# Kernel tuning notes

Hardware: AMD Instinct MI355X
Metric: run time of the kernel (lower is better)

The kernel has to match this reference:

```python
import jax, jax.numpy as jnp
import numpy as np

D = 256; HEADS = 8; LEVELS = 4; POINTS = 4; DFFN = 1024
B = 8; NQ = 300; NC = 16
SPATIAL = [(64, 64), (32, 32), (16, 16), (8, 8)]  # (H, W) per feature level (static)
LEN_IN = sum(h * w for h, w in SPATIAL)  # 5440
EPS = 1e-5


def layer_norm(x, w, b):
    m = x.mean(-1, keepdims=True)
    v = ((x - m) ** 2).mean(-1, keepdims=True)
    return (x - m) * jax.lax.rsqrt(v + EPS) * w + b


def mha(q, k, v, in_w, in_b, out_w, out_b):
    # torch nn.MultiheadAttention with packed qkv in_proj. q,k,v: [b, s, D]
    b, s, _ = q.shape
    dh = D // HEADS
    wq, wk, wv = jnp.split(in_w, 3, axis=0)
    bq, bk, bv = jnp.split(in_b, 3)
    proj = lambda x, w, bb: (x @ w.T + bb).reshape(b, s, HEADS, dh).transpose(0, 2, 1, 3)
    qh, kh, vh = proj(q, wq, bq), proj(k, wk, bk), proj(v, wv, bv)
    attn = jax.nn.softmax(jnp.einsum('bhqd,bhkd->bhqk', qh / np.sqrt(dh), kh), axis=-1)
    o = jnp.einsum('bhqk,bhkd->bhqd', attn, vh).transpose(0, 2, 1, 3).reshape(b, s, D)
    return o @ out_w.T + out_b


def bilinear_sample(value_l, loc, H_, W_):
    # value_l: [b, heads, H_*W_, dh]; loc: [b, heads, lq, P, 2] normalized to [0,1]
    # matches F.grid_sample(mode='bilinear', padding_mode='zeros', align_corners=False)
    b, nh, lq, p, _ = loc.shape
    dh = value_l.shape[-1]
    x = loc[..., 0] * W_ - 0.5
    y = loc[..., 1] * H_ - 0.5
    x0f = jnp.floor(x); y0f = jnp.floor(y)
    lx = x - x0f; ly = y - y0f
    x0 = x0f.astype(jnp.int32); y0 = y0f.astype(jnp.int32)
    def gather(xi, yi, w):
        valid = (xi >= 0) & (xi < W_) & (yi >= 0) & (yi < H_)
        idx = jnp.clip(yi, 0, H_ - 1) * W_ + jnp.clip(xi, 0, W_ - 1)
        vals = jnp.take_along_axis(value_l, idx.reshape(b, nh, lq * p, 1), axis=2)
        return vals.reshape(b, nh, lq, p, dh) * (w * valid)[..., None]
    out = gather(x0, y0, (1 - lx) * (1 - ly))
    out = out + gather(x0 + 1, y0, lx * (1 - ly))
    out = out + gather(x0, y0 + 1, (1 - lx) * ly)
    out = out + gather(x0 + 1, y0 + 1, lx * ly)
    return out  # [b, heads, lq, P, dh]


def ms_deform_attn(query, ref_pts, src, pad_mask, value_w, value_b, off_w, off_b, attw_w, attw_b, out_w, out_b):
    b, lq, _ = query.shape
    dh = D // HEADS
    value = src @ value_w.T + value_b
    value = jnp.where(pad_mask[..., None], 0.0, value)
    value = value.reshape(b, LEN_IN, HEADS, dh).transpose(0, 2, 1, 3)  # [b,H,Len,dh]
    off = (query @ off_w.T + off_b).reshape(b, lq, HEADS, LEVELS, POINTS, 2)
    aw = jax.nn.softmax((query @ attw_w.T + attw_b).reshape(b, lq, HEADS, LEVELS * POINTS), axis=-1)
    aw = aw.reshape(b, lq, HEADS, LEVELS, POINTS).transpose(0, 2, 1, 3, 4)  # [b,H,lq,L,P]
    norm = jnp.array([[w_, h_] for h_, w_ in SPATIAL], dtype=query.dtype)  # (W, H) per level
    loc = ref_pts[:, :, None, :, None, :] + off / norm[None, None, None, :, None, :]
    loc = loc.transpose(0, 2, 1, 3, 4, 5)  # [b,H,lq,L,P,2]
    out = jnp.zeros((b, HEADS, lq, dh), query.dtype)
    start = 0
    for l, (H_, W_) in enumerate(SPATIAL):
        v_l = jax.lax.dynamic_slice_in_dim(value, start, H_ * W_, axis=2)
        s = bilinear_sample(v_l, loc[:, :, :, l], H_, W_)
        out = out + (s * aw[:, :, :, l, :, None]).sum(3)
        start += H_ * W_
    out = out.transpose(0, 2, 1, 3).reshape(b, lq, D)
    return out @ out_w.T + out_b


def setup_inputs():
    ks = iter(jax.random.split(jax.random.key(0), 64))
    w = lambda *shape: jax.random.normal(next(ks), shape, jnp.float32) * 0.02
    return {
        'tgt': jax.random.normal(next(ks), (B, NQ, NC, D), jnp.float32),
        'query_pos': jax.random.normal(next(ks), (B, NQ, NC, D), jnp.float32),
        'reference_points': jax.random.uniform(next(ks), (B, NQ * NC, LEVELS, 2), jnp.float32),
        'src': jax.random.normal(next(ks), (B, LEN_IN, D), jnp.float32),
        'src_spatial_shapes': jnp.array(SPATIAL, jnp.int32),
        'level_start_index': jnp.array(np.cumsum([0] + [h * ww for h, ww in SPATIAL[:-1]]), jnp.int32),
        'src_padding_mask': jnp.zeros((B, LEN_IN), bool),
        'sa_in_w': w(3 * D, D), 'sa_in_b': jnp.zeros(3 * D, jnp.float32),
        'sa_out_w': w(D, D), 'sa_out_b': jnp.zeros(D, jnp.float32),
        'norm2_w': jnp.ones(D, jnp.float32), 'norm2_b': jnp.zeros(D, jnp.float32),
        'ca_value_w': w(D, D), 'ca_value_b': jnp.zeros(D, jnp.float32),
        'ca_off_w': w(HEADS * LEVELS * POINTS * 2, D), 'ca_off_b': w(HEADS * LEVELS * POINTS * 2),
        'ca_attw_w': w(HEADS * LEVELS * POINTS, D), 'ca_attw_b': jnp.zeros(HEADS * LEVELS * POINTS, jnp.float32),
        'ca_out_w': w(D, D), 'ca_out_b': jnp.zeros(D, jnp.float32),
        'norm1_w': jnp.ones(D, jnp.float32), 'norm1_b': jnp.zeros(D, jnp.float32),
        'lin1_w': w(DFFN, D), 'lin1_b': jnp.zeros(DFFN, jnp.float32),
        'lin2_w': w(D, DFFN), 'lin2_b': jnp.zeros(D, jnp.float32),
        'norm3_w': jnp.ones(D, jnp.float32), 'norm3_b': jnp.zeros(D, jnp.float32),
    }


def _forward(tgt, query_pos, reference_points, src, pad_mask, sa_in_w, sa_in_b, sa_out_w, sa_out_b, norm2_w, norm2_b, ca_value_w, ca_value_b, ca_off_w, ca_off_b, ca_attw_w, ca_attw_b, ca_out_w, ca_out_b, norm1_w, norm1_b, lin1_w, lin1_b, lin2_w, lin2_b, norm3_w, norm3_b):
    b, nq, nc, dm = tgt.shape
    # point-to-point self-attention within each contour (batch folded with queries)
    t = tgt.reshape(b * nq, nc, dm)
    qp = query_pos.reshape(b * nq, nc, dm)
    q = t + qp
    t2 = mha(q, q, t, sa_in_w, sa_in_b, sa_out_w, sa_out_b)
    t = layer_norm(t + t2, norm2_w, norm2_b)
    # multi-scale deformable cross-attention over flattened feature pyramid
    t = t.reshape(b, nq * nc, dm)
    qp = qp.reshape(b, nq * nc, dm)
    t2 = ms_deform_attn(t + qp, reference_points, src, pad_mask, ca_value_w, ca_value_b, ca_off_w, ca_off_b, ca_attw_w, ca_attw_b, ca_out_w, ca_out_b)
    t = layer_norm(t + t2, norm1_w, norm1_b)
    # FFN (dropout is identity in eval)
    t2 = jax.nn.relu(t @ lin1_w.T + lin1_b) @ lin2_w.T + lin2_b
    t = layer_norm(t + t2, norm3_w, norm3_b)
    return t.reshape(b, nq, nc, dm)


def reference(tgt, query_pos, reference_points, src, src_spatial_shapes, level_start_index, src_padding_mask, sa_in_w, sa_in_b, sa_out_w, sa_out_b, norm2_w, norm2_b, ca_value_w, ca_value_b, ca_off_w, ca_off_b, ca_attw_w, ca_attw_b, ca_out_w, ca_out_b, norm1_w, norm1_b, lin1_w, lin1_b, lin2_w, lin2_b, norm3_w, norm3_b):
    # src_spatial_shapes / level_start_index are static (SPATIAL); accepted for API fidelity
    return _forward(tgt, query_pos, reference_points, src, src_padding_mask, sa_in_w, sa_in_b, sa_out_w, sa_out_b, norm2_w, norm2_b, ca_value_w, ca_value_b, ca_off_w, ca_off_b, ca_attw_w, ca_attw_b, ca_out_w, ca_out_b, norm1_w, norm1_b, lin1_w, lin1_b, lin2_w, lin2_b, norm3_w, norm3_b)
```

## Files before the change

kernel.cpp:

```cpp
#include <hip/hip_runtime.h>


typedef __bf16 bf16x8 __attribute__((ext_vector_type(8)));
typedef float  f32x4  __attribute__((ext_vector_type(4)));
typedef float  f32x2  __attribute__((ext_vector_type(2)));

__device__ __forceinline__ unsigned pk_bf16(float lo, float hi)
{
    unsigned a = __float_as_uint(lo) + 0x8000u;
    unsigned b = __float_as_uint(hi) + 0x8000u;
    return __builtin_amdgcn_perm(b, a, 0x07060302u);
}
__device__ __forceinline__ unsigned short f2bf(float v)
{
    return (unsigned short)((__float_as_uint(v) + 0x8000u) >> 16);
}
__device__ __forceinline__ float bf_lo(unsigned u) { return __uint_as_float(u << 16); }
__device__ __forceinline__ float bf_hi(unsigned u) { return __uint_as_float(u & 0xffff0000u); }
__device__ __forceinline__ float bf1(unsigned short u) { return __uint_as_float((unsigned)u << 16); }
__device__ __forceinline__ f32x2 bfpair(unsigned u)
{
    f32x2 r;
    r.x = __uint_as_float(u << 16);
    r.y = __uint_as_float(u & 0xffff0000u);
    return r;
}

__device__ __forceinline__ int xcd_swz(int wgid, int nwg)
{
    const int q = nwg >> 3, r = nwg & 7;
    const int x = wgid & 7, k = wgid >> 3;
    return (x < r ? x * (q + 1) : r * (q + 1) + (x - r) * q) + k;
}

__device__ __forceinline__ void gl_lds16(const unsigned short* g, unsigned short* l)
{
    __builtin_amdgcn_global_load_lds(
        (const __attribute__((address_space(1))) unsigned int*)g,
        (__attribute__((address_space(3))) unsigned int*)l,
        16, 0, 0);
}

struct WcvtArgs {
    const float* src[8];
    unsigned short* dst[8];
    int n4[8];
};

__global__ __launch_bounds__(256) void wcvt(WcvtArgs a)
{
    const int gid = blockIdx.x * 256 + threadIdx.x;
    const int stride = gridDim.x * 256;
#pragma unroll
    for (int s = 0; s < 8; s++) {
        const float4* sp = (const float4*)a.src[s];
        uint2* dp = (uint2*)a.dst[s];
        for (int i = gid; i < a.n4[s]; i += stride) {
            float4 f = sp[i];
            uint2 o; o.x = pk_bf16(f.x, f.y); o.y = pk_bf16(f.z, f.w);
            dp[i] = o;
        }
    }
}

__global__ __launch_bounds__(256) void cvt_acts(
    const float* __restrict__ tgt, const float* __restrict__ qpos,
    const float* __restrict__ src,
    unsigned short* __restrict__ tgtB, unsigned short* __restrict__ qB,
    unsigned short* __restrict__ srcB)
{
    const int gid = blockIdx.x * 256 + threadIdx.x;
    const int stride = gridDim.x * 256;
    for (int i = gid; i < 2457600; i += stride) {
        float4 t = ((const float4*)tgt)[i];
        float4 p = ((const float4*)qpos)[i];
        uint2 a; a.x = pk_bf16(t.x, t.y); a.y = pk_bf16(t.z, t.w);
        ((uint2*)tgtB)[i] = a;
        uint2 b; b.x = pk_bf16(t.x + p.x, t.y + p.y);
        b.y = pk_bf16(t.z + p.z, t.w + p.w);
        ((uint2*)qB)[i] = b;
    }
    for (int i = gid; i < 2785280; i += stride) {
        float4 s = ((const float4*)src)[i];
        uint2 c; c.x = pk_bf16(s.x, s.y); c.y = pk_bf16(s.z, s.w);
        ((uint2*)srcB)[i] = c;
    }
}

__device__ __forceinline__ void gemm_core128(
    const unsigned short* __restrict__ Ab,
    const unsigned short* __restrict__ Wb, const float* __restrict__ bias,
    void* __restrict__ Cv, int outbf16, int relu,
    int row0, int col0, int N, int K,
    unsigned short (*sA)[128][32], unsigned short (*sB)[128][32])
{
    const int tid  = threadIdx.x;
    const int lane = tid & 63;
    const int wv   = tid >> 6;
    const int wr   = wv >> 1;
    const int wc   = wv & 1;
    const int lm   = lane & 15;
    const int q    = lane >> 4;
    const int q4   = q << 2;

    const int tr = tid >> 2;
    const int ts = tid & 3;

    f32x4 acc[4][4] = {};
    const int iters = K >> 5;

    auto stage = [&](int buf, int k) {
#pragma unroll
        for (int r = 0; r < 2; ++r) {
            const int row = r * 64 + tr;
            const int sw  = ts ^ ((row >> 1) & 3);
            gl_lds16(Ab + (size_t)(row0 + row) * K + k + sw * 8,
                     &sA[buf][0][0] + (size_t)(r * 256 + tid) * 8);
            gl_lds16(Wb + (size_t)(col0 + row) * K + k + sw * 8,
                     &sB[buf][0][0] + (size_t)(r * 256 + tid) * 8);
        }
    };

    stage(0, 0);

    for (int it = 0; it < iters; ++it) {
        __syncthreads();
        const int buf = it & 1;
        if (it + 1 < iters) stage(buf ^ 1, (it + 1) << 5);

        bf16x8 av[4], bv[4];
#pragma unroll
        for (int mi = 0; mi < 4; mi++) {
            const int row = wr * 64 + mi * 16 + lm;
            av[mi] = *(const bf16x8*)&sA[buf][row][(q ^ ((row >> 1) & 3)) * 8];
        }
#pragma unroll
        for (int ni = 0; ni < 4; ni++) {
            const int row = wc * 64 + ni * 16 + lm;
            bv[ni] = *(const bf16x8*)&sB[buf][row][(q ^ ((row >> 1) & 3)) * 8];
        }
#pragma unroll
        for (int mi = 0; mi < 4; mi++)
#pragma unroll
            for (int ni = 0; ni < 4; ni++)
                acc[mi][ni] = __builtin_amdgcn_mfma_f32_16x16x32_bf16(
                    av[mi], bv[ni], acc[mi][ni], 0, 0, 0);
    }

#pragma unroll
    for (int ni = 0; ni < 4; ni++) {
        const int col = col0 + wc * 64 + ni * 16 + lm;
        const float bsv = bias[col];
#pragma unroll
        for (int mi = 0; mi < 4; mi++) {
            const int rowb = row0 + wr * 64 + mi * 16 + q4;
#pragma unroll
            for (int rr = 0; rr < 4; rr++) {
                float v = acc[mi][ni][rr] + bsv;
                if (relu) v = fmaxf(v, 0.f);
                if (outbf16)
                    ((unsigned short*)Cv)[(size_t)(rowb + rr) * N + col] = f2bf(v);
                else
                    ((float*)Cv)[(size_t)(rowb + rr) * N + col] = v;
            }
        }
    }
}

__global__ __launch_bounds__(256) void gemm_std128(
    const unsigned short* __restrict__ Ab,
    const unsigned short* __restrict__ Wb, const float* __restrict__ bias,
    void* __restrict__ Cv, int outbf16, int relu, int N, int K)
{
    __shared__ unsigned short sA[2][128][32];
    __shared__ unsigned short sB[2][128][32];
    const int nwg = gridDim.x * gridDim.y;
    const int w = xcd_swz(blockIdx.x + gridDim.x * blockIdx.y, nwg);
    const int x = w % gridDim.x, y = w / gridDim.x;
    gemm_core128(Ab, Wb, bias, Cv, outbf16, relu,
                 y * 128, x * 128, N, K, sA, sB);
}

__global__ __launch_bounds__(256) void gemm_qkvval(
    const unsigned short* __restrict__ qB, const unsigned short* __restrict__ tgtB,
    const unsigned short* __restrict__ srcB,
    const unsigned short* __restrict__ Wsa, const float* __restrict__ bsa,
    unsigned short* __restrict__ qkB, unsigned short* __restrict__ vB,
    const unsigned short* __restrict__ Wval, const float* __restrict__ bval,
    unsigned short* __restrict__ valB)
{
    __shared__ unsigned short sA[2][128][32];
    __shared__ unsigned short sB[2][128][32];
    const int w = xcd_swz(blockIdx.x + 8 * blockIdx.y, 2720);
    const int x = w & 7, y = w >> 3;
    if (x < 4) {
        if (y >= 300) return;
        gemm_core128(qB, Wsa, bsa, qkB, 1, 0, y * 128, x * 128, 512, 256, sA, sB);
    } else if (x < 6) {
        if (y >= 300) return;
        gemm_core128(tgtB, Wsa + 512 * 256, bsa + 512, vB, 1, 0,
                     y * 128, (x - 4) * 128, 256, 256, sA, sB);
    } else {
        gemm_core128(srcB, Wval, bval, valB, 1, 0,
                     y * 128, (x - 6) * 128, 256, 256, sA, sB);
    }
}

__global__ __launch_bounds__(256) void gemm_offaw(
    const unsigned short* __restrict__ X,
    const unsigned short* __restrict__ Woff, const float* __restrict__ boff,
    unsigned short* __restrict__ offB,
    const unsigned short* __restrict__ Watt, const float* __restrict__ batt,
    float* __restrict__ awL)
{
    __shared__ unsigned short sA[2][128][32];
    __shared__ unsigned short sB[2][128][32];
    const int w = xcd_swz(blockIdx.x + 3 * blockIdx.y, 900);
    const int x = w % 3, y = w / 3;
    if (x >= 2)
        gemm_core128(X, Watt, batt, awL, 0, 0,
                     y * 128, 0, 128, 256, sA, sB);
    else
        gemm_core128(X, Woff, boff, offB, 1, 0,
                     y * 128, x * 128, 256, 256, sA, sB);
}

__global__ __launch_bounds__(256) void attn16(
    const unsigned short* __restrict__ QK, const unsigned short* __restrict__ V,
    unsigned short* __restrict__ O)
{
    __shared__ unsigned short sqk[16][520];
    __shared__ unsigned short sv[16][264];
    __shared__ float sp[128][17];

    const int g = blockIdx.x;
    const int tid = threadIdx.x;

    const uint4* qg = (const uint4*)(QK + (size_t)g * 8192);
    for (int i = tid; i < 1024; i += 256)
        *(uint4*)&sqk[i >> 6][(i & 63) * 8] = qg[i];
    const uint4* vg = (const uint4*)(V + (size_t)g * 4096);
    for (int i = tid; i < 512; i += 256)
        *(uint4*)&sv[i >> 5][(i & 31) * 8] = vg[i];
    __syncthreads();

#pragma unroll 2
    for (int s = tid; s < 2048; s += 256) {
        const int h = s >> 8, qi = (s >> 4) & 15, kj = s & 15;
        const uint4* qp = (const uint4*)&sqk[qi][h * 32];
        const uint4* kp = (const uint4*)&sqk[kj][256 + h * 32];
        float acc = 0.f;
#pragma unroll
        for (int c = 0; c < 4; c++) {
            uint4 qu = qp[c];
            uint4 ku = kp[c];
            acc += bf_lo(qu.x) * bf_lo(ku.x) + bf_hi(qu.x) * bf_hi(ku.x)
                 + bf_lo(qu.y) * bf_lo(ku.y) + bf_hi(qu.y) * bf_hi(ku.y)
                 + bf_lo(qu.z) * bf_lo(ku.z) + bf_hi(qu.z) * bf_hi(ku.z)
                 + bf_lo(qu.w) * bf_lo(ku.w) + bf_hi(qu.w) * bf_hi(ku.w);
        }
        sp[s >> 4][s & 15] = acc * 0.17677669529663687f;
    }
    __syncthreads();

    if (tid < 128) {
        float* row = sp[tid];
        float mx = row[0];
#pragma unroll
        for (int j = 1; j < 16; j++) mx = fmaxf(mx, row[j]);
        float sum = 0.f;
#pragma unroll
        for (int j = 0; j < 16; j++) { float e = __expf(row[j] - mx); row[j] = e; sum += e; }
        float inv = 1.f / sum;
#pragma unroll
        for (int j = 0; j < 16; j++) row[j] *= inv;
    }
    __syncthreads();

    uint2* og = (uint2*)(O + (size_t)g * 4096);
    for (int o = tid; o < 1024; o += 256) {
        const int qi = o >> 6, cq = o & 63, h = cq >> 3;
        const float* pr = sp[h * 16 + qi];
        float a0 = 0.f, a1 = 0.f, a2 = 0.f, a3 = 0.f;
#pragma unroll
        for (int j = 0; j < 16; j++) {
            uint2 u = *(const uint2*)&sv[j][cq * 4];
            float p = pr[j];
            a0 += p * bf_lo(u.x); a1 += p * bf_hi(u.x);
            a2 += p * bf_lo(u.y); a3 += p * bf_hi(u.y);
        }
        uint2 r; r.x = pk_bf16(a0, a1); r.y = pk_bf16(a2, a3);
        og[o] = r;
    }
}

template <int XBF16, int WRITE2, int ADDQ>
__global__ __launch_bounds__(256) void ln_res4(
    const void* __restrict__ Xv, const float* __restrict__ R,
    const float* __restrict__ w, const float* __restrict__ b,
    float* __restrict__ out, unsigned short* __restrict__ out2,
    const float* __restrict__ qpos)
{
    const int row = blockIdx.x * 4 + (threadIdx.x >> 6);
    const int lane = threadIdx.x & 63;
    const size_t base = (size_t)row * 256 + lane * 4;

    float x0, x1, x2, x3;
    if (XBF16) {
        uint2 u = *(const uint2*)((const unsigned short*)Xv + base);
        x0 = bf_lo(u.x); x1 = bf_hi(u.x); x2 = bf_lo(u.y); x3 = bf_hi(u.y);
    } else {
        float4 f = *(const float4*)((const float*)Xv + base);
        x0 = f.x; x1 = f.y; x2 = f.z; x3 = f.w;
    }
    float4 r4 = *(const float4*)&R[base];
    float v0 = x0 + r4.x, v1 = x1 + r4.y, v2 = x2 + r4.z, v3 = x3 + r4.w;

    float s = v0 + v1 + v2 + v3;
#pragma unroll
    for (int o = 32; o > 0; o >>= 1) s += __shfl_xor(s, o);
    const float mean = s * (1.f / 256.f);
    const float d0 = v0 - mean, d1 = v1 - mean, d2 = v2 - mean, d3 = v3 - mean;
    float qv = d0 * d0 + d1 * d1 + d2 * d2 + d3 * d3;
#pragma unroll
    for (int o = 32; o > 0; o >>= 1) qv += __shfl_xor(qv, o);
    const float rs = rsqrtf(qv * (1.f / 256.f) + 1e-5f);

    float4 w4 = *(const float4*)&w[lane * 4];
    float4 b4 = *(const float4*)&b[lane * 4];
    float y0 = d0 * rs * w4.x + b4.x;
    float y1 = d1 * rs * w4.y + b4.y;
    float y2 = d2 * rs * w4.z + b4.z;
    float y3 = d3 * rs * w4.w + b4.w;

    float4 o4; o4.x = y0; o4.y = y1; o4.z = y2; o4.w = y3;
    *(float4*)&out[base] = o4;
    if (WRITE2) {
        float z0 = y0, z1 = y1, z2 = y2, z3 = y3;
        if (ADDQ) {
            float4 qp4 = *(const float4*)&qpos[base];
            z0 += qp4.x; z1 += qp4.y; z2 += qp4.z; z3 += qp4.w;
        }
        uint2 u; u.x = pk_bf16(z0, z1); u.y = pk_bf16(z2, z3);
        *(uint2*)(out2 + base) = u;
    }
}

__global__ __launch_bounds__(256) void ms_sample3(
    const unsigned short* __restrict__ VAL, const unsigned short* __restrict__ OFF,
    const float* __restrict__ AWL, const float* __restrict__ REF,
    unsigned short* __restrict__ OUT)
{
    __shared__ char smem[24576];
    unsigned short* soff = (unsigned short*)smem;
    float*          saw  = (float*)(smem + 4096);
    float*          sref = (float*)(smem + 8192);
    float*          swt  = (float*)smem;
    unsigned short* sidx = (unsigned short*)(smem + 16384);

    const int wblk = xcd_swz(blockIdx.x, 4800);
    const int m0 = wblk * 8, tid = threadIdx.x;

    ((uint4*)soff)[tid]  = ((const uint4*)(OFF + (size_t)m0 * 256))[tid];
    ((float4*)saw)[tid]  = ((const float4*)(AWL + (size_t)m0 * 128))[tid];
    if (tid < 64) sref[tid] = REF[(size_t)m0 * 8 + tid];
    __syncthreads();

    {
        const int row = tid >> 2, part = tid & 3;
        float4 lg = *(float4*)&saw[row * 16 + part * 4];
        float mx = fmaxf(fmaxf(lg.x, lg.y), fmaxf(lg.z, lg.w));
        mx = fmaxf(mx, __shfl_xor(mx, 1));
        mx = fmaxf(mx, __shfl_xor(mx, 2));
        float e0 = __expf(lg.x - mx), e1 = __expf(lg.y - mx);
        float e2 = __expf(lg.z - mx), e3 = __expf(lg.w - mx);
        float s = e0 + e1 + e2 + e3;
        s += __shfl_xor(s, 1);
        s += __shfl_xor(s, 2);
        const float inv = 1.f / s;
        float4 pr; pr.x = e0 * inv; pr.y = e1 * inv; pr.z = e2 * inv; pr.w = e3 * inv;
        *(float4*)&saw[row * 16 + part * 4] = pr;
    }
    __syncthreads();

    float4  w4r[4];
    ushort4 rr[4];
#pragma unroll
    for (int k = 0; k < 4; k++) {
        const int c = tid + k * 256;
        const int qi = c >> 7, h = c & 7, j = (c >> 3) & 15;
        const int l = j >> 2, p = j & 3;
        const int Wl = 64 >> l;
        const int st = (l == 0) ? 0 : (l == 1) ? 4096 : (l == 2) ? 5120 : 5376;
        const float fS = (float)Wl;
        const unsigned short* ob = &soff[qi * 256 + h * 32 + l * 8 + p * 2];
        const float x = sref[qi * 8 + l * 2 + 0] * fS + bf1(ob[0]) - 0.5f;
        const float y = sref[qi * 8 + l * 2 + 1] * fS + bf1(ob[1]) - 0.5f;
        const float x0f = floorf(x), y0f = floorf(y);
        const float fx = x - x0f, fy = y - y0f;
        const int x0 = (int)x0f, y0 = (int)y0f;
        const int x1 = x0 + 1, y1 = y0 + 1;
        const float vx0 = (x0 >= 0 && x0 < Wl) ? 1.f : 0.f;
        const float vx1 = (x1 >= 0 && x1 < Wl) ? 1.f : 0.f;
        const float vy0 = (y0 >= 0 && y0 < Wl) ? 1.f : 0.f;
        const float vy1 = (y1 >= 0 && y1 < Wl) ? 1.f : 0.f;
        const int cx0 = min(max(x0, 0), Wl - 1);
        const int cx1 = min(max(x1, 0), Wl - 1);
        const int cy0 = min(max(y0, 0), Wl - 1);
        const int cy1 = min(max(y1, 0), Wl - 1);
        const float aw = saw[qi * 128 + h * 16 + j];
        w4r[k].x = (1.f - fx) * (1.f - fy) * vx0 * vy0 * aw;
        w4r[k].y = fx * (1.f - fy) * vx1 * vy0 * aw;
        w4r[k].z = (1.f - fx) * fy * vx0 * vy1 * aw;
        w4r[k].w = fx * fy * vx1 * vy1 * aw;
        rr[k].x = (unsigned short)(st + cy0 * Wl + cx0);
        rr[k].y = (unsigned short)(st + cy0 * Wl + cx1);
        rr[k].z = (unsigned short)(st + cy1 * Wl + cx0);
        rr[k].w = (unsigned short)(st + cy1 * Wl + cx1);
    }
    __syncthreads();

#pragma unroll
    for (int k = 0; k < 4; k++) {
        const int c = tid + k * 256;
        const int qi = c >> 7, h = c & 7, j = (c >> 3) & 15;
        *(float4*)&swt[((qi * 16 + j) * 8 + h) * 4]  = w4r[k];
        *(ushort4*)&sidx[((qi * 16 + j) * 8 + h) * 4] = rr[k];
    }
    __syncthreads();

    const int qi = tid >> 5;
    const int l31 = tid & 31;
    const int h = l31 >> 2;
    const unsigned loff = (unsigned)l31 * 16;
    const int m = m0 + qi;
    const char* vbase = (const char*)VAL + (size_t)(m0 / 4800) * 5440 * 512;

    f32x2 a0 = {0.f, 0.f}, a1 = {0.f, 0.f}, a2 = {0.f, 0.f}, a3 = {0.f, 0.f};
#pragma unroll 8
    for (int j = 0; j < 16; j++) {
        const float4  w  = *(const float4*)&swt[((qi * 16 + j) * 8 + h) * 4];
        const ushort4 rw = *(const ushort4*)&sidx[((qi * 16 + j) * 8 + h) * 4];
        const uint4 c0 = *(const uint4*)(vbase + (((unsigned)rw.x << 9) + loff));
        const uint4 c1 = *(const uint4*)(vbase + (((unsigned)rw.y << 9) + loff));
        const uint4 c2 = *(const uint4*)(vbase + (((unsigned)rw.z << 9) + loff));
        const uint4 c3 = *(const uint4*)(vbase + (((unsigned)rw.w << 9) + loff));
        a0 += w.x * bfpair(c0.x); a1 += w.x * bfpair(c0.y);
        a2 += w.x * bfpair(c0.z); a3 += w.x * bfpair(c0.w);
        a0 += w.y * bfpair(c1.x); a1 += w.y * bfpair(c1.y);
        a2 += w.y * bfpair(c1.z); a3 += w.y * bfpair(c1.w);
        a0 += w.z * bfpair(c2.x); a1 += w.z * bfpair(c2.y);
        a2 += w.z * bfpair(c2.z); a3 += w.z * bfpair(c2.w);
        a0 += w.w * bfpair(c3.x); a1 += w.w * bfpair(c3.y);
        a2 += w.w * bfpair(c3.z); a3 += w.w * bfpair(c3.w);
    }
    uint4 o;
    o.x = pk_bf16(a0.x, a0.y);
    o.y = pk_bf16(a1.x, a1.y);
    o.z = pk_bf16(a2.x, a2.y);
    o.w = pk_bf16(a3.x, a3.y);
    *(uint4*)(OUT + (size_t)m * 256 + l31 * 8) = o;
}

extern "C" void kernel_launch(void* const* d_in, const int* in_sizes, int n_in,
                              void* d_out, int out_size, void* d_ws, size_t ws_size,
                              hipStream_t stream)
{
    const float* tgt        = (const float*)d_in[0];
    const float* qpos       = (const float*)d_in[1];
    const float* refp       = (const float*)d_in[2];
    const float* src        = (const float*)d_in[3];
    const float* sa_in_w    = (const float*)d_in[7];
    const float* sa_in_b    = (const float*)d_in[8];
    const float* sa_out_w   = (const float*)d_in[9];
    const float* sa_out_b   = (const float*)d_in[10];
    const float* norm2_w    = (const float*)d_in[11];
    const float* norm2_b    = (const float*)d_in[12];
    const float* ca_value_w = (const float*)d_in[13];
    const float* ca_value_b = (const float*)d_in[14];
    const float* ca_off_w   = (const float*)d_in[15];
    const float* ca_off_b   = (const float*)d_in[16];
    const float* ca_attw_w  = (const float*)d_in[17];
    const float* ca_attw_b  = (const float*)d_in[18];
    const float* ca_out_w   = (const float*)d_in[19];
    const float* ca_out_b   = (const float*)d_in[20];
    const float* norm1_w    = (const float*)d_in[21];
    const float* norm1_b    = (const float*)d_in[22];
    const float* lin1_w     = (const float*)d_in[23];
    const float* lin1_b     = (const float*)d_in[24];
    const float* lin2_w     = (const float*)d_in[25];
    const float* lin2_b     = (const float*)d_in[26];
    const float* norm3_w    = (const float*)d_in[27];
    const float* norm3_b    = (const float*)d_in[28];
    float* out = (float*)d_out;

    float* ws = (float*)d_ws;
    float* A  = ws;
    float* Bx = A  + 9830400;
    float* Cx = Bx + 4915200;
    float* Dx = Cx + 4915200;
    float* Ex = Dx + 4915200;
    float* Fx = Ex + 5570560;
    float* Gx = Fx + 19660800;

    unsigned short* qkB   = (unsigned short*)A;
    float*          t1    = A;
    float*          t2    = A;
    unsigned short* vB    = (unsigned short*)Bx;
    unsigned short* t1qB  = (unsigned short*)Bx;
    unsigned short* sampB = (unsigned short*)Bx;
    unsigned short* l2B   = (unsigned short*)Bx;
    unsigned short* aoB   = (unsigned short*)Cx;
    unsigned short* offB  = (unsigned short*)Cx;
    unsigned short* coB   = (unsigned short*)Cx;
    unsigned short* t2B   = (unsigned short*)Cx;
    unsigned short* soB   = (unsigned short*)Dx;
    float*          awL   = Dx;
    unsigned short* valB  = (unsigned short*)Ex;
    unsigned short* hidB  = (unsigned short*)Fx;
    unsigned short* wG    = (unsigned short*)Gx;

    unsigned short* qBa   = (unsigned short*)Fx;
    unsigned short* tgtBa = qBa + 9830400;
    unsigned short* srcBa = tgtBa + 9830400;

    unsigned short* wSAIN  = wG;
    unsigned short* wSAOUT = wG + 196608;
    unsigned short* wVAL   = wG + 262144;
    unsigned short* wOFF   = wG + 327680;
    unsigned short* wATT   = wG + 393216;
    unsigned short* wCAOUT = wG + 425984;
    unsigned short* wL1    = wG + 491520;
    unsigned short* wL2    = wG + 753664;

    dim3 blk(256);

    WcvtArgs wa;
    wa.src[0] = sa_in_w;    wa.dst[0] = wSAIN;  wa.n4[0] = 196608 / 4;
    wa.src[1] = sa_out_w;   wa.dst[1] = wSAOUT; wa.n4[1] = 65536 / 4;
    wa.src[2] = ca_value_w; wa.dst[2] = wVAL;   wa.n4[2] = 65536 / 4;
    wa.src[3] = ca_off_w;   wa.dst[3] = wOFF;   wa.n4[3] = 65536 / 4;
    wa.src[4] = ca_attw_w;  wa.dst[4] = wATT;   wa.n4[4] = 32768 / 4;
    wa.src[5] = ca_out_w;   wa.dst[5] = wCAOUT; wa.n4[5] = 65536 / 4;
    wa.src[6] = lin1_w;     wa.dst[6] = wL1;    wa.n4[6] = 262144 / 4;
    wa.src[7] = lin2_w;     wa.dst[7] = wL2;    wa.n4[7] = 262144 / 4;
    wcvt<<<512, blk, 0, stream>>>(wa);
    cvt_acts<<<2048, blk, 0, stream>>>(tgt, qpos, src, tgtBa, qBa, srcBa);

    gemm_qkvval<<<dim3(8, 340), blk, 0, stream>>>(qBa, tgtBa, srcBa, wSAIN, sa_in_b,
                                                  qkB, vB, wVAL, ca_value_b, valB);
    attn16<<<2400, blk, 0, stream>>>(qkB, vB, aoB);
    gemm_std128<<<dim3(2, 300), blk, 0, stream>>>(aoB, wSAOUT, sa_out_b, soB, 1, 0, 256, 256);
    ln_res4<1, 1, 1><<<9600, blk, 0, stream>>>(soB, tgt, norm2_w, norm2_b, t1, t1qB, qpos);

    gemm_offaw<<<dim3(3, 300), blk, 0, stream>>>(t1qB, wOFF, ca_off_b, offB, wATT, ca_attw_b, awL);
    ms_sample3<<<4800, blk, 0, stream>>>(valB, offB, awL, refp, sampB);
    gemm_std128<<<dim3(2, 300), blk, 0, stream>>>(sampB, wCAOUT, ca_out_b, coB, 1, 0, 256, 256);
    ln_res4<1, 1, 0><<<9600, blk, 0, stream>>>(coB, t1, norm1_w, norm1_b, t2, t2B, nullptr);

    gemm_std128<<<dim3(8, 300), blk, 0, stream>>>(t2B, wL1, lin1_b, hidB, 1, 1, 1024, 256);
    gemm_std128<<<dim3(2, 300), blk, 0, stream>>>(hidB, wL2, lin2_b, l2B, 1, 0, 256, 1024);
    ln_res4<1, 0, 0><<<9600, blk, 0, stream>>>(l2B, t2, norm3_w, norm3_b, out, nullptr, nullptr);
}
```

Baseline: 541.3 us.

## Fuse residual LayerNorm into output GEMMs and software-pipeline deformable sampling gathers

Adds a 64-row by 256-column GEMM kernel that computes the full output row per block, then applies bias, residual add and LayerNorm in its epilogue, optionally writing a bf16 copy with query_pos added. It replaces three GEMM+ln_res4 pairs, so the bf16 intermediates are no longer written and re-read and three launches disappear. The sampling kernel now prefetches the next point's weights and four value gathers before accumulating the current point, to hide gather latency. The fused GEMM uses smaller M tiles (600 blocks) and single-pass variance, and its epilogue does scalar strided stores and reads the residual inside the reduction loop.

```diff
diff --git a/kernel.cpp b/kernel.cpp
--- a/kernel.cpp
+++ b/kernel.cpp
@@ -225,6 +225,146 @@
                      y * 128, x * 128, 256, 256, sA, sB);
 }
 
+template <int WRITE2, int ADDQ>
+__global__ __launch_bounds__(256) void gemm_ln64(
+    const unsigned short* __restrict__ Ab,
+    const unsigned short* __restrict__ Wb,
+    const float* __restrict__ bias,
+    const float* __restrict__ R,
+    const float* __restrict__ lnw, const float* __restrict__ lnb,
+    float* __restrict__ outF,
+    unsigned short* __restrict__ out2,
+    const float* __restrict__ qpos,
+    int K, int nblk)
+{
+    __shared__ unsigned short sA[2][64][32];
+    __shared__ unsigned short sB[2][256][32];
+    __shared__ float red[64][10];
+
+    const int wblk = xcd_swz(blockIdx.x, nblk);
+    const int row0 = wblk * 64;
+
+    const int tid  = threadIdx.x;
+    const int lane = tid & 63;
+    const int wc   = tid >> 6;
+    const int lm   = lane & 15;
+    const int q    = lane >> 4;
+    const int q4   = q << 2;
+
+    const int tr = tid >> 2;
+    const int ts = tid & 3;
+
+    f32x4 acc[4][4] = {};
+    const int iters = K >> 5;
+
+    auto stage = [&](int buf, int k) {
+        {
+            const int row = tr;
+            const int sw  = ts ^ ((row >> 1) & 3);
+            gl_lds16(Ab + (size_t)(row0 + row) * K + k + sw * 8,
+                     &sA[buf][0][0] + (size_t)tid * 8);
+        }
+#pragma unroll
+        for (int r = 0; r < 4; ++r) {
+            const int row = r * 64 + tr;
+            const int sw  = ts ^ ((row >> 1) & 3);
+            gl_lds16(Wb + (size_t)row * K + k + sw * 8,
+                     &sB[buf][0][0] + (size_t)(r * 256 + tid) * 8);
+        }
+    };
+
+    stage(0, 0);
+
+    for (int it = 0; it < iters; ++it) {
+        __syncthreads();
+        const int buf = it & 1;
+        if (it + 1 < iters) stage(buf ^ 1, (it + 1) << 5);
+
+        bf16x8 av[4], bv[4];
+#pragma unroll
+        for (int mi = 0; mi < 4; mi++) {
+            const int row = mi * 16 + lm;
+            av[mi] = *(const bf16x8*)&sA[buf][row][(q ^ ((row >> 1) & 3)) * 8];
+        }
+#pragma unroll
+        for (int ni = 0; ni < 4; ni++) {
+            const int row = wc * 64 + ni * 16 + lm;
+            bv[ni] = *(const bf16x8*)&sB[buf][row][(q ^ ((row >> 1) & 3)) * 8];
+        }
+#pragma unroll
+        for (int mi = 0; mi < 4; mi++)
+#pragma unroll
+            for (int ni = 0; ni < 4; ni++)
+                acc[mi][ni] = __builtin_amdgcn_mfma_f32_16x16x32_bf16(
+                    av[mi], bv[ni], acc[mi][ni], 0, 0, 0);
+    }
+    __syncthreads();
+
+    const int colb = wc * 64;
+    float bsv[4];
+#pragma unroll
+    for (int ni = 0; ni < 4; ni++) bsv[ni] = bias[colb + ni * 16 + lm];
+
+#pragma unroll
+    for (int mi = 0; mi < 4; mi++) {
+#pragma unroll
+        for (int rr = 0; rr < 4; rr++) {
+            const int lr = mi * 16 + q4 + rr;
+            const size_t gb = (size_t)(row0 + lr) * 256 + colb + lm;
+            float s = 0.f, sq = 0.f;
+#pragma unroll
+            for (int ni = 0; ni < 4; ni++) {
+                float v = acc[mi][ni][rr] + bsv[ni] + R[gb + ni * 16];
+                acc[mi][ni][rr] = v;
+                s += v; sq += v * v;
+            }
+#pragma unroll
+            for (int o = 1; o < 16; o <<= 1) {
+                s  += __shfl_xor(s, o);
+                sq += __shfl_xor(sq, o);
+            }
+            if (lm == 0) { red[lr][wc] = s; red[lr][4 + wc] = sq; }
+        }
+    }
+    __syncthreads();
+
+    if (tid < 64) {
+        float s  = red[tid][0] + red[tid][1] + red[tid][2] + red[tid][3];
+        float sq = red[tid][4] + red[tid][5] + red[tid][6] + red[tid][7];
+        float mean = s * (1.f / 256.f);
+        float var  = sq * (1.f / 256.f) - mean * mean;
+        red[tid][8] = mean;
+        red[tid][9] = rsqrtf(fmaxf(var, 0.f) + 1e-5f);
+    }
+    __syncthreads();
+
+    float w4v[4], b4v[4];
+#pragma unroll
+    for (int ni = 0; ni < 4; ni++) {
+        w4v[ni] = lnw[colb + ni * 16 + lm];
+        b4v[ni] = lnb[colb + ni * 16 + lm];
+    }
+#pragma unroll
+    for (int mi = 0; mi < 4; mi++) {
+#pragma unroll
+        for (int rr = 0; rr < 4; rr++) {
+            const int lr = mi * 16 + q4 + rr;
+            const float mean = red[lr][8], rs = red[lr][9];
+            const size_t gb = (size_t)(row0 + lr) * 256 + colb + lm;
+#pragma unroll
+            for (int ni = 0; ni < 4; ni++) {
+                const float y = (acc[mi][ni][rr] - mean) * rs * w4v[ni] + b4v[ni];
+                outF[gb + ni * 16] = y;
+                if (WRITE2) {
+                    float z = y;
+                    if (ADDQ) z += qpos[gb + ni * 16];
+                    out2[gb + ni * 16] = f2bf(z);
+                }
+            }
+        }
+    }
+}
+
 __global__ __launch_bounds__(256) void attn16(
     const unsigned short* __restrict__ QK, const unsigned short* __restrict__ V,
     unsigned short* __restrict__ O)
@@ -294,59 +434,7 @@
     }
 }
 
-template <int XBF16, int WRITE2, int ADDQ>
-__global__ __launch_bounds__(256) void ln_res4(
-    const void* __restrict__ Xv, const float* __restrict__ R,
-    const float* __restrict__ w, const float* __restrict__ b,
-    float* __restrict__ out, unsigned short* __restrict__ out2,
-    const float* __restrict__ qpos)
-{
-    const int row = blockIdx.x * 4 + (threadIdx.x >> 6);
-    const int lane = threadIdx.x & 63;
-    const size_t base = (size_t)row * 256 + lane * 4;
-
-    float x0, x1, x2, x3;
-    if (XBF16) {
-        uint2 u = *(const uint2*)((const unsigned short*)Xv + base);
-        x0 = bf_lo(u.x); x1 = bf_hi(u.x); x2 = bf_lo(u.y); x3 = bf_hi(u.y);
-    } else {
-        float4 f = *(const float4*)((const float*)Xv + base);
-        x0 = f.x; x1 = f.y; x2 = f.z; x3 = f.w;
-    }
-    float4 r4 = *(const float4*)&R[base];
-    float v0 = x0 + r4.x, v1 = x1 + r4.y, v2 = x2 + r4.z, v3 = x3 + r4.w;
-
-    float s = v0 + v1 + v2 + v3;
-#pragma unroll
-    for (int o = 32; o > 0; o >>= 1) s += __shfl_xor(s, o);
-    const float mean = s * (1.f / 256.f);
-    const float d0 = v0 - mean, d1 = v1 - mean, d2 = v2 - mean, d3 = v3 - mean;
-    float qv = d0 * d0 + d1 * d1 + d2 * d2 + d3 * d3;
-#pragma unroll
-    for (int o = 32; o > 0; o >>= 1) qv += __shfl_xor(qv, o);
-    const float rs = rsqrtf(qv * (1.f / 256.f) + 1e-5f);
-
-    float4 w4 = *(const float4*)&w[lane * 4];
-    float4 b4 = *(const float4*)&b[lane * 4];
-    float y0 = d0 * rs * w4.x + b4.x;
-    float y1 = d1 * rs * w4.y + b4.y;
-    float y2 = d2 * rs * w4.z + b4.z;
-    float y3 = d3 * rs * w4.w + b4.w;
-
-    float4 o4; o4.x = y0; o4.y = y1; o4.z = y2; o4.w = y3;
-    *(float4*)&out[base] = o4;
-    if (WRITE2) {
-        float z0 = y0, z1 = y1, z2 = y2, z3 = y3;
-        if (ADDQ) {
-            float4 qp4 = *(const float4*)&qpos[base];
-            z0 += qp4.x; z1 += qp4.y; z2 += qp4.z; z3 += qp4.w;
-        }
-        uint2 u; u.x = pk_bf16(z0, z1); u.y = pk_bf16(z2, z3);
-        *(uint2*)(out2 + base) = u;
-    }
-}
-
-__global__ __launch_bounds__(256) void ms_sample3(
+__global__ __launch_bounds__(256) void ms_sample4p(
     const unsigned short* __restrict__ VAL, const unsigned short* __restrict__ OFF,
     const float* __restrict__ AWL, const float* __restrict__ REF,
     unsigned short* __restrict__ OUT)
@@ -384,7 +472,7 @@
     __syncthreads();
 
     float4  w4r[4];
-    ushort4 rr[4];
+    ushort4 rr4[4];
 #pragma unroll
     for (int k = 0; k < 4; k++) {
         const int c = tid + k * 256;
@@ -413,10 +501,10 @@
         w4r[k].y = fx * (1.f - fy) * vx1 * vy0 * aw;
         w4r[k].z = (1.f - fx) * fy * vx0 * vy1 * aw;
         w4r[k].w = fx * fy * vx1 * vy1 * aw;
-        rr[k].x = (unsigned short)(st + cy0 * Wl + cx0);
-        rr[k].y = (unsigned short)(st + cy0 * Wl + cx1);
-        rr[k].z = (unsigned short)(st + cy1 * Wl + cx0);
-        rr[k].w = (unsigned short)(st + cy1 * Wl + cx1);
+        rr4[k].x = (unsigned short)(st + cy0 * Wl + cx0);
+        rr4[k].y = (unsigned short)(st + cy0 * Wl + cx1);
+        rr4[k].z = (unsigned short)(st + cy1 * Wl + cx0);
+        rr4[k].w = (unsigned short)(st + cy1 * Wl + cx1);
     }
     __syncthreads();
 
@@ -424,8 +512,8 @@
     for (int k = 0; k < 4; k++) {
         const int c = tid + k * 256;
         const int qi = c >> 7, h = c & 7, j = (c >> 3) & 15;
-        *(float4*)&swt[((qi * 16 + j) * 8 + h) * 4]  = w4r[k];
-        *(ushort4*)&sidx[((qi * 16 + j) * 8 + h) * 4] = rr[k];
+        *(float4*)&swt[((qi * 16 + j) * 8 + h) * 4]   = w4r[k];
+        *(ushort4*)&sidx[((qi * 16 + j) * 8 + h) * 4] = rr4[k];
     }
     __syncthreads();
 
@@ -435,16 +523,28 @@
     const unsigned loff = (unsigned)l31 * 16;
     const int m = m0 + qi;
     const char* vbase = (const char*)VAL + (size_t)(m0 / 4800) * 5440 * 512;
+    const int sbase = qi * 512 + h * 4;
+
+    float4  w  = *(const float4*)&swt[sbase];
+    ushort4 rw = *(const ushort4*)&sidx[sbase];
+    uint4 c0 = *(const uint4*)(vbase + (((unsigned)rw.x << 9) + loff));
+    uint4 c1 = *(const uint4*)(vbase + (((unsigned)rw.y << 9) + loff));
+    uint4 c2 = *(const uint4*)(vbase + (((unsigned)rw.z << 9) + loff));
+    uint4 c3 = *(const uint4*)(vbase + (((unsigned)rw.w << 9) + loff));
 
     f32x2 a0 = {0.f, 0.f}, a1 = {0.f, 0.f}, a2 = {0.f, 0.f}, a3 = {0.f, 0.f};
-#pragma unroll 8
+#pragma unroll
     for (int j = 0; j < 16; j++) {
-        const float4  w  = *(const float4*)&swt[((qi * 16 + j) * 8 + h) * 4];
-        const ushort4 rw = *(const ushort4*)&sidx[((qi * 16 + j) * 8 + h) * 4];
-        const uint4 c0 = *(const uint4*)(vbase + (((unsigned)rw.x << 9) + loff));
-        const uint4 c1 = *(const uint4*)(vbase + (((unsigned)rw.y << 9) + loff));
-        const uint4 c2 = *(const uint4*)(vbase + (((unsigned)rw.z << 9) + loff));
-        const uint4 c3 = *(const uint4*)(vbase + (((unsigned)rw.w << 9) + loff));
+        float4 wn = w; uint4 n0 = c0, n1 = c1, n2 = c2, n3 = c3;
+        if (j < 15) {
+            const int nb = sbase + (j + 1) * 32;
+            wn = *(const float4*)&swt[nb];
+            const ushort4 rn = *(const ushort4*)&sidx[nb];
+            n0 = *(const uint4*)(vbase + (((unsigned)rn.x << 9) + loff));
+            n1 = *(const uint4*)(vbase + (((unsigned)rn.y << 9) + loff));
+            n2 = *(const uint4*)(vbase + (((unsigned)rn.z << 9) + loff));
+            n3 = *(const uint4*)(vbase + (((unsigned)rn.w << 9) + loff));
+        }
         a0 += w.x * bfpair(c0.x); a1 += w.x * bfpair(c0.y);
         a2 += w.x * bfpair(c0.z); a3 += w.x * bfpair(c0.w);
         a0 += w.y * bfpair(c1.x); a1 += w.y * bfpair(c1.y);
@@ -453,6 +553,7 @@
         a2 += w.z * bfpair(c2.z); a3 += w.z * bfpair(c2.w);
         a0 += w.w * bfpair(c3.x); a1 += w.w * bfpair(c3.y);
         a2 += w.w * bfpair(c3.z); a3 += w.w * bfpair(c3.w);
+        w = wn; c0 = n0; c1 = n1; c2 = n2; c3 = n3;
     }
     uint4 o;
     o.x = pk_bf16(a0.x, a0.y);
@@ -509,12 +610,9 @@
     unsigned short* vB    = (unsigned short*)Bx;
     unsigned short* t1qB  = (unsigned short*)Bx;
     unsigned short* sampB = (unsigned short*)Bx;
-    unsigned short* l2B   = (unsigned short*)Bx;
     unsigned short* aoB   = (unsigned short*)Cx;
     unsigned short* offB  = (unsigned short*)Cx;
-    unsigned short* coB   = (unsigned short*)Cx;
     unsigned short* t2B   = (unsigned short*)Cx;
-    unsigned short* soB   = (unsigned short*)Dx;
     float*          awL   = Dx;
     unsigned short* valB  = (unsigned short*)Ex;
     unsigned short* hidB  = (unsigned short*)Fx;
@@ -550,15 +648,18 @@
     gemm_qkvval<<<dim3(8, 340), blk, 0, stream>>>(qBa, tgtBa, srcBa, wSAIN, sa_in_b,
                                                   qkB, vB, wVAL, ca_value_b, valB);
     attn16<<<2400, blk, 0, stream>>>(qkB, vB, aoB);
-    gemm_std128<<<dim3(2, 300), blk, 0, stream>>>(aoB, wSAOUT, sa_out_b, soB, 1, 0, 256, 256);
-    ln_res4<1, 1, 1><<<9600, blk, 0, stream>>>(soB, tgt, norm2_w, norm2_b, t1, t1qB, qpos);
+    gemm_ln64<1, 1><<<600, blk, 0, stream>>>(aoB, wSAOUT, sa_out_b, tgt,
+                                             norm2_w, norm2_b, t1, t1qB, qpos,
+                                             256, 600);
 
     gemm_offaw<<<dim3(3, 300), blk, 0, stream>>>(t1qB, wOFF, ca_off_b, offB, wATT, ca_attw_b, awL);
-    ms_sample3<<<4800, blk, 0, stream>>>(valB, offB, awL, refp, sampB);
-    gemm_std128<<<dim3(2, 300), blk, 0, stream>>>(sampB, wCAOUT, ca_out_b, coB, 1, 0, 256, 256);
-    ln_res4<1, 1, 0><<<9600, blk, 0, stream>>>(coB, t1, norm1_w, norm1_b, t2, t2B, nullptr);
+    ms_sample4p<<<4800, blk, 0, stream>>>(valB, offB, awL, refp, sampB);
+    gemm_ln64<1, 0><<<600, blk, 0, stream>>>(sampB, wCAOUT, ca_out_b, t1,
+                                             norm1_w, norm1_b, t2, t2B, nullptr,
+                                             256, 600);
 
     gemm_std128<<<dim3(8, 300), blk, 0, stream>>>(t2B, wL1, lin1_b, hidB, 1, 1, 1024, 256);
-    gemm_std128<<<dim3(2, 300), blk, 0, stream>>>(hidB, wL2, lin2_b, l2B, 1, 0, 256, 1024);
-    ln_res4<1, 0, 0><<<9600, blk, 0, stream>>>(l2B, t2, norm3_w, norm3_b, out, nullptr, nullptr);
-}
+    gemm_ln64<0, 0><<<600, blk, 0, stream>>>(hidB, wL2, lin2_b, t2,
+                                             norm3_w, norm3_b, out, nullptr, nullptr,
+                                             1024, 600);
+}
```

Result: slower. 662.2 us (+22.3%).
